# Kernel optimization log

Hardware: AMD Instinct MI355X
Metric: run time of the kernel (lower is better)

The kernel has to match this reference:

```python
import jax, jax.numpy as jnp
import numpy as np

B, A, N_IN, N_POINTS = 64, 256, 512, 2048


def _sq_cdist(u, v):
    # |u_i - v_j|^2 via expansion, abs() as in the torch original
    d = -2.0 * (u @ v.T) + (u * u).sum(1)[:, None] + (v * v).sum(1)[None, :]
    return jnp.abs(d)


def setup_inputs() -> dict:
    key = jax.random.key(0)
    k1, k2, k3, k4 = jax.random.split(key, 4)
    x = jax.random.normal(k1, (B, A, N_IN), dtype=jnp.float32)
    atom_mask = jax.random.bernoulli(k2, 0.8, (B, A))  # ragged valid-atom mask
    inducing_points = jax.random.normal(k3, (N_POINTS, N_IN), dtype=jnp.float32)
    gamma = (1.0 + 0.25 * jax.random.normal(k4, (N_IN,), dtype=jnp.float32)) * np.sqrt(N_IN).astype(np.float32)
    return {"x": x, "atom_mask": atom_mask, "inducing_points": inducing_points, "gamma": gamma}


def reference(x, atom_mask, inducing_points, gamma):
    b, a, n_in = x.shape
    m = atom_mask.astype(x.dtype)                      # [B, A]
    mf = m[..., None]                                  # [B, A, 1]
    n = m.sum()
    # masked mean / unbiased std over valid atoms (torch .std is ddof=1)
    mean = (x * mf).sum((0, 1)) / n                    # [n_in]
    var = (((x - mean) ** 2) * mf).sum((0, 1)) / (n - 1.0)
    std = jnp.sqrt(var) + 1e-5                         # [n_in]
    xn = (x - mean) / std * mf                         # zero out padded atoms

    g2 = gamma ** 2 + 0.001                            # [n_in]
    z = (xn / g2).reshape(b * a, n_in)                 # [N, n_in]
    zi = inducing_points / g2                          # [M, n_in]

    Kx = jnp.exp(-_sq_cdist(z, zi))                    # [N, M]
    Kind = jnp.exp(-_sq_cdist(zi, zi))                 # [M, M]
    Kinv = jnp.linalg.inv(Kind + 0.05 * jnp.eye(Kind.shape[0], dtype=x.dtype))

    t = Kx @ Kinv                                      # [N, M]
    x_new = ((t @ inducing_points) * std + mean).reshape(b, a, n_in) * mf
    var_out = (1.0 - (t * Kx).sum(-1)).reshape(b, a) * m
    return x_new, var_out
```

## Files before the change

### kernel.cpp

```cpp
#include <hip/hip_runtime.h>
#include <math.h>
#include <stdint.h>

namespace {

constexpr int NROW = 16384;
constexpr int NF   = 512;
constexpr int MIND = 2048;
constexpr float CC = 0.98f;

typedef _Float16 half8 __attribute__((ext_vector_type(8)));
typedef _Float16 half4v __attribute__((ext_vector_type(4)));
typedef float floatx4 __attribute__((ext_vector_type(4)));

__device__ __forceinline__ void gload16(const void* g, void* l) {
  __builtin_amdgcn_global_load_lds(
      (__attribute__((address_space(1))) void*)g,
      (__attribute__((address_space(3))) void*)l, 16, 0, 0);
}

#define MEMFENCE asm volatile("" ::: "memory")
#define GATE(N) asm volatile("s_waitcnt vmcnt(" #N ")" ::: "memory")

__global__ __launch_bounds__(256) void stats_kernel(
    const float* __restrict__ x, const int* __restrict__ mask,
    float* __restrict__ sum, float* __restrict__ sumsq, float* __restrict__ cnt)
{
  const int t = threadIdx.x;
  const int row0 = blockIdx.x * 64;
  float s0 = 0.f, s1 = 0.f, q0 = 0.f, q1 = 0.f, c = 0.f;
  for (int r = 0; r < 64; ++r) {
    const int row = row0 + r;
    const float m = (mask[row] != 0) ? 1.f : 0.f;
    const float v0 = x[(size_t)row * NF + t];
    const float v1 = x[(size_t)row * NF + t + 256];
    s0 += m * v0; q0 += m * v0 * v0;
    s1 += m * v1; q1 += m * v1 * v1;
    c += m;
  }
  atomicAdd(&sum[t], s0);        atomicAdd(&sum[t + 256], s1);
  atomicAdd(&sumsq[t], q0);      atomicAdd(&sumsq[t + 256], q1);
  if (t == 0) atomicAdd(cnt, c);
}

__global__ __launch_bounds__(256) void finalize_stats(
    const float* __restrict__ sum, const float* __restrict__ sumsq,
    const float* __restrict__ cnt, const float* __restrict__ gamma,
    float* __restrict__ meanv, float* __restrict__ stdv,
    float* __restrict__ zsv, float* __restrict__ giv)
{
  const int f = blockIdx.x * 256 + threadIdx.x;
  const float n = cnt[0];
  const float mu = sum[f] / n;
  const float var = (sumsq[f] - sum[f] * mu) / (n - 1.0f);
  const float sd = sqrtf(var) + 1e-5f;
  const float g = gamma[f];
  const float g2 = g * g + 0.001f;
  meanv[f] = mu;
  stdv[f]  = sd;
  zsv[f]   = 1.0f / (sd * g2);
  giv[f]   = 1.0f / g2;
}

__global__ __launch_bounds__(256) void make_z(
    const float* __restrict__ x, const int* __restrict__ mask,
    const float* __restrict__ ip, const float* __restrict__ meanv,
    const float* __restrict__ zsv, const float* __restrict__ giv,
    _Float16* __restrict__ Zh, _Float16* __restrict__ Zih,
    float* __restrict__ rnorm, float* __restrict__ cnorm)
{
  const int row = blockIdx.x;
  const int t = threadIdx.x;
  float v0, v1;
  if (row < NROW) {
    const float m = (mask[row] != 0) ? 1.f : 0.f;
    v0 = (x[(size_t)row * NF + t      ] - meanv[t      ]) * zsv[t      ] * m;
    v1 = (x[(size_t)row * NF + t + 256] - meanv[t + 256]) * zsv[t + 256] * m;
    const _Float16 h0 = (_Float16)v0, h1 = (_Float16)v1;
    Zh[(size_t)row * NF + t] = h0;
    Zh[(size_t)row * NF + t + 256] = h1;
    v0 = (float)h0; v1 = (float)h1;
  } else {
    const int r = row - NROW;
    v0 = ip[(size_t)r * NF + t      ] * giv[t      ];
    v1 = ip[(size_t)r * NF + t + 256] * giv[t + 256];
    const _Float16 h0 = (_Float16)v0, h1 = (_Float16)v1;
    Zih[(size_t)r * NF + t] = h0;
    Zih[(size_t)r * NF + t + 256] = h1;
    v0 = (float)h0; v1 = (float)h1;
  }
  float nrm = v0 * v0 + v1 * v1;
  #pragma unroll
  for (int off = 32; off; off >>= 1) nrm += __shfl_xor(nrm, off);
  __shared__ float red[4];
  if ((t & 63) == 0) red[t >> 6] = nrm;
  __syncthreads();
  if (t == 0) {
    const float s = red[0] + red[1] + red[2] + red[3];
    if (row < NROW) rnorm[row] = s; else cnorm[row - NROW] = s;
  }
}

__global__ __launch_bounds__(256) void ip_t16(
    const float* __restrict__ ip, _Float16* __restrict__ ipTh)
{
  __shared__ float T[64][65];
  const int j0 = blockIdx.x * 64;
  const int f0 = blockIdx.y * 64;
  const int t = threadIdx.x;
  #pragma unroll
  for (int l = 0; l < 16; ++l) {
    const int idx = t + l * 256;
    T[idx >> 6][idx & 63] = ip[(size_t)(j0 + (idx >> 6)) * NF + f0 + (idx & 63)];
  }
  __syncthreads();
  #pragma unroll
  for (int l = 0; l < 16; ++l) {
    const int idx = t + l * 256;
    const int fr = idx >> 6, jc = idx & 63;
    ipTh[(size_t)(f0 + fr) * MIND + j0 + jc] = (_Float16)T[jc][fr];
  }
}

template <int PASS>
__global__ __launch_bounds__(512, 2) void mfma_gemm256f(
    const _Float16* __restrict__ A, const _Float16* __restrict__ B, int K,
    const float* __restrict__ rn, const float* __restrict__ cn,
    _Float16* __restrict__ DKout, float* __restrict__ Cf,
    const _Float16* __restrict__ DK, const float* __restrict__ u,
    float* __restrict__ varacc,
    const float* __restrict__ colsumR, const float* __restrict__ stdv,
    const float* __restrict__ meanv, const int* __restrict__ mask)
{
  __shared__ __align__(16) _Float16 Asmem[4][256 * 32];
  __shared__ __align__(16) _Float16 Bsmem[4][256 * 32];

  const int tid = threadIdx.x;
  const int w = tid >> 6, L = tid & 63;
  const int wm = w >> 2, wn = w & 3;
  const int lq = L >> 4, lr = L & 15;
  int bn, bm;
  if constexpr (PASS == 0) {
    const int wgid = blockIdx.y * 8 + blockIdx.x;
    const int xcd = wgid & 7, q = wgid >> 3;
    bm = xcd + 8 * (q >> 3);
    bn = q & 7;
  } else if constexpr (PASS == 1) {
    const int wgid = blockIdx.y * 10 + blockIdx.x;
    const int xcd = wgid & 7, q = wgid >> 3;
    bm = xcd + 8 * (q / 10);
    bn = q % 10;
  } else {
    const int wgid = blockIdx.y * 8 + blockIdx.x;
    bm = wgid >> 3;
    bn = wgid & 7;
  }
  const int NT = K >> 5;

  const int srow  = tid >> 2;
  const int sslot = tid & 3;
  const int gslot = sslot ^ ((tid >> 3) & 3);
  const _Float16* Ag = A + (size_t)(bm * 256 + srow) * K + gslot * 8;
  const _Float16* Bg = B + (size_t)(bn * 256 + srow) * K + gslot * 8;
  const size_t rstride = (size_t)128 * K;
  const int ldst = srow * 32 + sslot * 8;

  const int fswz = (lq ^ ((lr >> 1) & 3)) * 8;
  const int aoff = (wm * 128 + lr) * 32 + fswz;
  const int boff = (wn * 64  + lr) * 32 + fswz;

  floatx4 acc[8][4] = {};

  auto stageA = [&](int t) {
    _Float16* dst = Asmem[t & 3] + ldst;
    const _Float16* src = Ag + (size_t)t * 32;
    gload16(src, dst);
    gload16(src + rstride, dst + 128 * 32);
  };
  auto stageB = [&](int t) {
    _Float16* dst = Bsmem[t & 3] + ldst;
    const _Float16* src = Bg + (size_t)t * 32;
    gload16(src, dst);
    gload16(src + rstride, dst + 128 * 32);
  };

  stageA(0); stageB(0);
  if (NT > 1) { stageA(1); stageB(1); }
  if (NT > 2) { stageA(2); stageB(2); }
  if (NT > 2)      { GATE(8); }
  else if (NT > 1) { GATE(4); }
  else             { GATE(0); }
  __builtin_amdgcn_s_barrier();
  MEMFENCE;

  for (int t = 0; t < NT; ++t) {
    const _Float16* As = Asmem[t & 3];
    const _Float16* Bs = Bsmem[t & 3];
    half8 af[4], bf[4], af2[4];

    #pragma unroll
    for (int mi = 0; mi < 4; ++mi) af[mi] = *(const half8*)&As[aoff + mi * 512];
    #pragma unroll
    for (int ni = 0; ni < 4; ++ni) bf[ni] = *(const half8*)&Bs[boff + ni * 512];
    if (t + 3 < NT) stageA(t + 3);
    MEMFENCE;
    __builtin_amdgcn_s_barrier();
    MEMFENCE;
    __builtin_amdgcn_s_setprio(1);
    #pragma unroll
    for (int mi = 0; mi < 4; ++mi)
      #pragma unroll
      for (int ni = 0; ni < 4; ++ni)
        acc[mi][ni] = __builtin_amdgcn_mfma_f32_16x16x32_f16(
            af[mi], bf[ni], acc[mi][ni], 0, 0, 0);
    __builtin_amdgcn_s_setprio(0);

    #pragma unroll
    for (int mi = 0; mi < 4; ++mi)
      af2[mi] = *(const half8*)&As[aoff + (mi + 4) * 512];
    if (t + 3 < NT) stageB(t + 3);
    if (t + 4 <= NT)      { GATE(8); }
    else if (t + 3 == NT) { GATE(4); }
    else if (t + 2 == NT) { GATE(0); }
    __builtin_amdgcn_s_barrier();
    MEMFENCE;
    __builtin_amdgcn_s_setprio(1);
    #pragma unroll
    for (int mi = 0; mi < 4; ++mi)
      #pragma unroll
      for (int ni = 0; ni < 4; ++ni)
        acc[mi + 4][ni] = __builtin_amdgcn_mfma_f32_16x16x32_f16(
            af2[mi], bf[ni], acc[mi + 4][ni], 0, 0, 0);
    __builtin_amdgcn_s_setprio(0);
  }

  const int grb = bm * 256 + wm * 128;
  const int gcb = bn * 256 + wn * 64;

  if constexpr (PASS == 0) {
    if (bm < NROW / 256) {
      #pragma unroll
      for (int mi = 0; mi < 8; ++mi)
        #pragma unroll
        for (int e = 0; e < 4; ++e) {
          const int gr = grb + mi * 16 + lq * 4 + e;
          const float rni = rn[gr];
          #pragma unroll
          for (int ni = 0; ni < 4; ++ni) {
            const int gc = gcb + ni * 16 + lr;
            const float d = rni + cn[gc] - 2.f * acc[mi][ni][e];
            DKout[(size_t)gr * MIND + gc] = (_Float16)(expf(-fabsf(d)) - CC);
          }
        }
    } else {
      #pragma unroll
      for (int mi = 0; mi < 8; ++mi)
        #pragma unroll
        for (int e = 0; e < 4; ++e) {
          const int gr = grb + mi * 16 + lq * 4 + e;
          const int gr2 = gr - NROW;
          const float rni = rn[gr];
          #pragma unroll
          for (int ni = 0; ni < 4; ++ni) {
            const int gc = gcb + ni * 16 + lr;
            const float d = rni + cn[gc] - 2.f * acc[mi][ni][e];
            float kx = expf(-fabsf(d));
            if (gr2 == gc) kx += 0.05f;
            Cf[(size_t)gr2 * MIND + gc] = kx;
          }
        }
    }
  } else if constexpr (PASS == 1) {
    if (bn < MIND / 256) {
      #pragma unroll
      for (int mi = 0; mi < 8; ++mi)
        #pragma unroll
        for (int e = 0; e < 4; ++e) {
          const int gr = grb + mi * 16 + lq * 4 + e;
          float partial = 0.f;
          #pragma unroll
          for (int ni = 0; ni < 4; ++ni) {
            const int gc = gcb + ni * 16 + lr;
            const float tv = acc[mi][ni][e] + CC * u[gc];
            partial += tv * (CC + (float)DK[(size_t)gr * MIND + gc]);
          }
          partial += __shfl_xor(partial, 1);
          partial += __shfl_xor(partial, 2);
          partial += __shfl_xor(partial, 4);
          partial += __shfl_xor(partial, 8);
          if (lr == 0) atomicAdd(&varacc[gr], partial);
        }
    } else {
      const int gcb3 = (bn - MIND / 256) * 256 + wn * 64;
      #pragma unroll
      for (int mi = 0; mi < 8; ++mi)
        #pragma unroll
        for (int e = 0; e < 4; ++e) {
          const int gr = grb + mi * 16 + lq * 4 + e;
          const float mrow = (mask[gr] != 0) ? 1.f : 0.f;
          #pragma unroll
          for (int ni = 0; ni < 4; ++ni) {
            const int gc3 = gcb3 + ni * 16 + lr;
            const float v = acc[mi][ni][e] + CC * colsumR[gc3];
            Cf[(size_t)gr * NF + gc3] = (v * stdv[gc3] + meanv[gc3]) * mrow;
          }
        }
    }
  } else {
    #pragma unroll
    for (int mi = 0; mi < 8; ++mi)
      #pragma unroll
      for (int e = 0; e < 4; ++e) {
        const int gr = grb + mi * 16 + lq * 4 + e;
        #pragma unroll
        for (int ni = 0; ni < 4; ++ni) {
          const int gc = gcb + ni * 16 + lr;
          DKout[(size_t)gr * MIND + gc] = (_Float16)acc[mi][ni][e];
        }
      }
  }
}


__global__ __launch_bounds__(256) void gj_diag(
    float* __restrict__ A, float* __restrict__ Pall, int k)
{
  const int o = k * 64;
  __shared__ float D[64][68];
  const int t = threadIdx.x;
  #pragma unroll
  for (int l = 0; l < 4; ++l) {
    const int v = t + l * 256;
    const int r = v >> 4, c4 = (v & 15) << 2;
    *(float4*)&D[r][c4] = *(const float4*)(A + (size_t)(o + r) * MIND + o + c4);
  }
  __syncthreads();
  const int i = t >> 2, c0 = (t & 3) * 16;
  for (int s = 0; s < 64; ++s) {
    const float p = 1.0f / D[s][s];
    if (t < 64 && t != s) D[s][t] *= p;
    __syncthreads();
    if (i != s) {
      const float f = D[i][s];
      #pragma unroll
      for (int c = c0; c < c0 + 16; c += 4) {
        float4 ds = *(const float4*)&D[s][c];
        float4 di = *(const float4*)&D[i][c];
        di.x -= f * ds.x; di.y -= f * ds.y; di.z -= f * ds.z; di.w -= f * ds.w;
        *(float4*)&D[i][c] = di;
      }
      if (s >= c0 && s < c0 + 16) D[i][s] = -f * p;
    }
    if (t == 0) D[s][s] = p;
    __syncthreads();
  }
  float* P = Pall + k * 4096;
  #pragma unroll
  for (int l = 0; l < 4; ++l) {
    const int v = t + l * 256;
    const int r = v >> 4, c4 = (v & 15) << 2;
    const float4 dv = *(const float4*)&D[r][c4];
    *(float4*)(P + r * 64 + c4) = dv;
    *(float4*)(A + (size_t)(o + r) * MIND + o + c4) = dv;
  }
}

__global__ __launch_bounds__(256) void gj_prep(
    const float* __restrict__ A, const float* __restrict__ Pall,
    float* __restrict__ CP, float* __restrict__ Bsave, int k)
{
  const int o = k * 64;
  const int t = threadIdx.x;
  if (blockIdx.x >= 32) {
    const int j0 = (blockIdx.x - 32) * 64;
    #pragma unroll
    for (int l = 0; l < 4; ++l) {
      const int v = t + l * 256;
      const int r = v >> 4, c4 = (v & 15) << 2;
      *(float4*)(Bsave + r * MIND + j0 + c4) =
          *(const float4*)(A + (size_t)(o + r) * MIND + j0 + c4);
    }
    return;
  }
  const int i0 = blockIdx.x * 64;
  if (i0 == o) return;
  const float* P = Pall + k * 4096;
  __shared__ float At[64][68];
  __shared__ float Pl[64][68];
  #pragma unroll
  for (int l = 0; l < 4; ++l) {
    const int v = t + l * 256;
    const int r = v >> 4, c4 = (v & 15) << 2;
    const float4 av = *(const float4*)(A + (size_t)(i0 + r) * MIND + o + c4);
    At[c4 + 0][r] = av.x; At[c4 + 1][r] = av.y;
    At[c4 + 2][r] = av.z; At[c4 + 3][r] = av.w;
    *(float4*)&Pl[r][c4] = *(const float4*)(P + r * 64 + c4);
  }
  __syncthreads();
  const int ty = t >> 4, tx = t & 15;
  float acc[4][4] = {};
  for (int s = 0; s < 64; ++s) {
    const float4 a4 = *(const float4*)&At[s][ty * 4];
    const float4 b4 = *(const float4*)&Pl[s][tx * 4];
    const float a[4] = {a4.x, a4.y, a4.z, a4.w};
    const float b[4] = {b4.x, b4.y, b4.z, b4.w};
    #pragma unroll
    for (int i = 0; i < 4; ++i)
      #pragma unroll
      for (int j = 0; j < 4; ++j) acc[i][j] += a[i] * b[j];
  }
  #pragma unroll
  for (int i = 0; i < 4; ++i) {
    float4 o4; o4.x = acc[i][0]; o4.y = acc[i][1]; o4.z = acc[i][2]; o4.w = acc[i][3];
    *(float4*)(CP + (i0 + ty * 4 + i) * 64 + tx * 4) = o4;
  }
}

__global__ __launch_bounds__(256) void gj_apply(
    float* __restrict__ A, float* __restrict__ Pall,
    const float* __restrict__ CP, const float* __restrict__ Bsave, int k)
{
  const int o = k * 64;
  const int i0 = blockIdx.y * 64, j0 = blockIdx.x * 64;
  const int t = threadIdx.x;

  if (i0 == o && j0 == o) return;

  if (j0 == o) {
    #pragma unroll
    for (int l = 0; l < 4; ++l) {
      const int v = t + l * 256;
      const int r = v >> 4, c4 = (v & 15) << 2;
      float4 x = *(const float4*)(CP + (i0 + r) * 64 + c4);
      x.x = -x.x; x.y = -x.y; x.z = -x.z; x.w = -x.w;
      *(float4*)(A + (size_t)(i0 + r) * MIND + o + c4) = x;
    }
    return;
  }

  __shared__ float S1[64 * 68];
  __shared__ float S2[64 * 68];
  #define DD(r, c) S1[(r) * 68 + (c)]

  const bool isrow = (i0 == o);
  const float* Lsrc = isrow ? (Pall + k * 4096) : (CP + i0 * 64);
  #pragma unroll
  for (int l = 0; l < 4; ++l) {
    const int v = t + l * 256;
    const int r = v >> 4, c4 = (v & 15) << 2;
    const float4 lv = *(const float4*)(Lsrc + r * 64 + c4);
    S1[(c4 + 0) * 68 + r] = lv.x; S1[(c4 + 1) * 68 + r] = lv.y;
    S1[(c4 + 2) * 68 + r] = lv.z; S1[(c4 + 3) * 68 + r] = lv.w;
    *(float4*)&S2[r * 68 + c4] = *(const float4*)(Bsave + r * MIND + j0 + c4);
  }
  __syncthreads();
  const int ty = t >> 4, tx = t & 15;
  float acc[4][4] = {};
  for (int s = 0; s < 64; ++s) {
    const float4 a4 = *(const float4*)&S1[s * 68 + ty * 4];
    const float4 b4 = *(const float4*)&S2[s * 68 + tx * 4];
    const float a[4] = {a4.x, a4.y, a4.z, a4.w};
    const float b[4] = {b4.x, b4.y, b4.z, b4.w};
    #pragma unroll
    for (int i = 0; i < 4; ++i)
      #pragma unroll
      for (int j = 0; j < 4; ++j) acc[i][j] += a[i] * b[j];
  }

  if (isrow) {
    #pragma unroll
    for (int i = 0; i < 4; ++i) {
      float4 o4; o4.x = acc[i][0]; o4.y = acc[i][1]; o4.z = acc[i][2]; o4.w = acc[i][3];
      *(float4*)(A + (size_t)(o + ty * 4 + i) * MIND + j0 + tx * 4) = o4;
    }
    return;
  }

  const bool isdiagnext = (i0 == o + 64) && (j0 == o + 64);
  if (!isdiagnext) {
    #pragma unroll
    for (int i = 0; i < 4; ++i) {
      float* cp = A + (size_t)(i0 + ty * 4 + i) * MIND + j0 + tx * 4;
      float4 cv = *(const float4*)cp;
      cv.x -= acc[i][0]; cv.y -= acc[i][1]; cv.z -= acc[i][2]; cv.w -= acc[i][3];
      *(float4*)cp = cv;
    }
    return;
  }

  __syncthreads();
  #pragma unroll
  for (int i = 0; i < 4; ++i) {
    const float4 cv = *(const float4*)(A + (size_t)(i0 + ty * 4 + i) * MIND + j0 + tx * 4);
    DD(ty * 4 + i, tx * 4 + 0) = cv.x - acc[i][0];
    DD(ty * 4 + i, tx * 4 + 1) = cv.y - acc[i][1];
    DD(ty * 4 + i, tx * 4 + 2) = cv.z - acc[i][2];
    DD(ty * 4 + i, tx * 4 + 3) = cv.w - acc[i][3];
  }
  __syncthreads();
  const int di = t >> 2, c0 = (t & 3) * 16;
  for (int s = 0; s < 64; ++s) {
    const float p = 1.0f / DD(s, s);
    if (t < 64 && t != s) DD(s, t) *= p;
    __syncthreads();
    if (di != s) {
      const float f = DD(di, s);
      #pragma unroll
      for (int c = c0; c < c0 + 16; c += 4) {
        float4 ds = *(const float4*)&DD(s, c);
        float4 dv = *(const float4*)&DD(di, c);
        dv.x -= f * ds.x; dv.y -= f * ds.y; dv.z -= f * ds.z; dv.w -= f * ds.w;
        *(float4*)&DD(di, c) = dv;
      }
      if (s >= c0 && s < c0 + 16) DD(di, s) = -f * p;
    }
    if (t == 0) DD(s, s) = p;
    __syncthreads();
  }
  float* Pn = Pall + (k + 1) * 4096;
  #pragma unroll
  for (int l = 0; l < 4; ++l) {
    const int v = t + l * 256;
    const int r = v >> 4, c4 = (v & 15) << 2;
    const float4 dv = *(const float4*)&DD(r, c4);
    *(float4*)(Pn + r * 64 + c4) = dv;
    *(float4*)(A + (size_t)(i0 + r) * MIND + j0 + c4) = dv;
  }
  #undef DD
}

__global__ __launch_bounds__(256) void rowsum_cast(
    const float* __restrict__ Ai, float* __restrict__ u,
    _Float16* __restrict__ Kih)
{
  const int row = blockIdx.x * 4 + (threadIdx.x >> 6);
  const int lane = threadIdx.x & 63;
  const float* src = Ai + (size_t)row * MIND;
  _Float16* dst = Kih + (size_t)row * MIND;
  float s = 0.f;
  #pragma unroll
  for (int it = 0; it < 8; ++it) {
    const int c = it * 256 + lane * 4;
    const float4 v = *(const float4*)(src + c);
    s += v.x + v.y + v.z + v.w;
    half4v h; h.x = (_Float16)v.x; h.y = (_Float16)v.y;
    h.z = (_Float16)v.z; h.w = (_Float16)v.w;
    *(half4v*)(dst + c) = h;
  }
  #pragma unroll
  for (int off = 32; off; off >>= 1) s += __shfl_xor(s, off);
  if (lane == 0) u[row] = s;
}

__global__ __launch_bounds__(256) void colsum_u(
    const float* __restrict__ ip, const float* __restrict__ u,
    float* __restrict__ cs)
{
  const int b = blockIdx.x;
  const int t = threadIdx.x;
  float s0 = 0.f, s1 = 0.f;
  for (int r = 0; r < 64; ++r) {
    const int row = b * 64 + r;
    const float uk = u[row];
    s0 += uk * ip[(size_t)row * NF + t];
    s1 += uk * ip[(size_t)row * NF + t + 256];
  }
  atomicAdd(&cs[t], s0); atomicAdd(&cs[t + 256], s1);
}

__global__ __launch_bounds__(256) void var_finalize(
    const float* __restrict__ varacc, const int* __restrict__ mask,
    float* __restrict__ outv)
{
  const int i = blockIdx.x * 256 + threadIdx.x;
  const float m = (mask[i] != 0) ? 1.f : 0.f;
  outv[i] = (1.0f - varacc[i]) * m;
}

}

extern "C" void kernel_launch(void* const* d_in, const int* in_sizes, int n_in,
                              void* d_out, int out_size, void* d_ws, size_t ws_size,
                              hipStream_t stream)
{
  (void)in_sizes; (void)n_in; (void)out_size; (void)ws_size;
  const float* x     = (const float*)d_in[0];
  const int*   mask  = (const int*)d_in[1];
  const float* ip    = (const float*)d_in[2];
  const float* gamma = (const float*)d_in[3];
  float* out = (float*)d_out;

  float* w       = (float*)d_ws;
  float* sum     = w;
  float* sumsq   = w + 512;
  float* cnt     = w + 1024;
  float* varacc  = w + 1536;
  float* colsumR = w + 17920;
  float* meanv   = w + 18432;
  float* stdv    = w + 18944;
  float* zsv     = w + 19456;
  float* giv     = w + 19968;
  float* rnorm   = w + 20480;
  float* cnorm   = w + 36864;
  float* u       = w + 38912;
  float* Ai      = w + 40960;
  _Float16* ipTh = (_Float16*)(w + 4235264);
  float* Pall    = w + 5283840;
  float* CP      = w + 5414912;
  float* Bsave   = w + 5545984;
  _Float16* hb   = (_Float16*)(w + 5677056);
  _Float16* Zh   = hb;
  _Float16* Zih  = hb + 8388608;
  _Float16* DK   = hb + 9437184;
  _Float16* Kih  = hb + 42991616;
  _Float16* Rt   = hb + 47185920;

  hipMemsetAsync(w, 0, 18432 * sizeof(float), stream);

  stats_kernel<<<256, 256, 0, stream>>>(x, mask, sum, sumsq, cnt);
  finalize_stats<<<2, 256, 0, stream>>>(sum, sumsq, cnt, gamma, meanv, stdv, zsv, giv);
  make_z<<<NROW + MIND, 256, 0, stream>>>(x, mask, ip, meanv, zsv, giv, Zh, Zih, rnorm, cnorm);
  ip_t16<<<dim3(MIND / 64, NF / 64), 256, 0, stream>>>(ip, ipTh);

  mfma_gemm256f<0><<<dim3(MIND / 256, (NROW + MIND) / 256), 512, 0, stream>>>(
      Zh, Zih, NF, rnorm, cnorm,
      DK, Ai, nullptr, nullptr, nullptr, nullptr, nullptr, nullptr, nullptr);

  gj_diag<<<1, 256, 0, stream>>>(Ai, Pall, 0);
  gj_prep<<<64, 256, 0, stream>>>(Ai, Pall, CP, Bsave, 0);
  for (int k = 0; k < 32; ++k) {
    gj_apply<<<dim3(32, 32), 256, 0, stream>>>(Ai, Pall, CP, Bsave, k);
    if (k < 31) gj_prep<<<64, 256, 0, stream>>>(Ai, Pall, CP, Bsave, k + 1);
  }

  rowsum_cast<<<MIND / 4, 256, 0, stream>>>(Ai, u, Kih);
  mfma_gemm256f<2><<<dim3(8, 2), 512, 0, stream>>>(
      ipTh, Kih, MIND, nullptr, nullptr,
      Rt, nullptr, nullptr, nullptr, nullptr, nullptr, nullptr, nullptr, nullptr);
  colsum_u<<<MIND / 64, 256, 0, stream>>>(ip, u, colsumR);

  mfma_gemm256f<1><<<dim3((MIND + NF) / 256, NROW / 256), 512, 0, stream>>>(
      DK, Kih, MIND, nullptr, nullptr,
      nullptr, out, DK, u, varacc, colsumR, stdv, meanv, mask);

  var_finalize<<<NROW / 256, 256, 0, stream>>>(varacc, mask, out + (size_t)NROW * NF);
}
```

Before: 2.032 ms.

## Fuse Gauss-Jordan prep into apply with tile flags and merge small kernels

Folds the next step's pivot-panel prep into each Gauss-Jordan apply launch. Extra blocks spin on per-tile release/acquire flags until the tiles they need are ready, and the CP/Bsave buffers are double-buffered so reads and writes do not collide. This removes 31 separate prep launches and their serialization. It also folds stats finalization and the ip transpose into make_z, and folds the colsum into the small GEMM launch as extra blocks. The spin-wait relies on the producer blocks being scheduled alongside or before the waiting ones, which risks stalls or deadlock.

```diff
diff --git a/kernel.cpp b/kernel.cpp
--- a/kernel.cpp
+++ b/kernel.cpp
@@ -43,47 +43,65 @@
   if (t == 0) atomicAdd(cnt, c);
 }
 
-__global__ __launch_bounds__(256) void finalize_stats(
-    const float* __restrict__ sum, const float* __restrict__ sumsq,
-    const float* __restrict__ cnt, const float* __restrict__ gamma,
-    float* __restrict__ meanv, float* __restrict__ stdv,
-    float* __restrict__ zsv, float* __restrict__ giv)
-{
-  const int f = blockIdx.x * 256 + threadIdx.x;
-  const float n = cnt[0];
-  const float mu = sum[f] / n;
-  const float var = (sumsq[f] - sum[f] * mu) / (n - 1.0f);
-  const float sd = sqrtf(var) + 1e-5f;
-  const float g = gamma[f];
-  const float g2 = g * g + 0.001f;
-  meanv[f] = mu;
-  stdv[f]  = sd;
-  zsv[f]   = 1.0f / (sd * g2);
-  giv[f]   = 1.0f / g2;
-}
-
 __global__ __launch_bounds__(256) void make_z(
     const float* __restrict__ x, const int* __restrict__ mask,
-    const float* __restrict__ ip, const float* __restrict__ meanv,
-    const float* __restrict__ zsv, const float* __restrict__ giv,
+    const float* __restrict__ ip, const float* __restrict__ sum,
+    const float* __restrict__ sumsq, const float* __restrict__ cnt,
+    const float* __restrict__ gamma,
     _Float16* __restrict__ Zh, _Float16* __restrict__ Zih,
-    float* __restrict__ rnorm, float* __restrict__ cnorm)
-{
+    float* __restrict__ rnorm, float* __restrict__ cnorm,
+    float* __restrict__ meanv, float* __restrict__ stdv,
+    _Float16* __restrict__ ipTh)
+{
+  __shared__ float T[64][65];
   const int row = blockIdx.x;
   const int t = threadIdx.x;
+
+  if (row >= NROW + MIND) {
+    const int idx2 = row - (NROW + MIND);
+    const int j0 = (idx2 & 31) * 64, f0 = (idx2 >> 5) * 64;
+    #pragma unroll
+    for (int l = 0; l < 16; ++l) {
+      const int idx = t + l * 256;
+      T[idx >> 6][idx & 63] = ip[(size_t)(j0 + (idx >> 6)) * NF + f0 + (idx & 63)];
+    }
+    __syncthreads();
+    #pragma unroll
+    for (int l = 0; l < 16; ++l) {
+      const int idx = t + l * 256;
+      const int fr = idx >> 6, jc = idx & 63;
+      ipTh[(size_t)(f0 + fr) * MIND + j0 + jc] = (_Float16)T[jc][fr];
+    }
+    return;
+  }
+
+  const float n = cnt[0];
+  float mu[2], zs[2], gi[2];
+  #pragma unroll
+  for (int h = 0; h < 2; ++h) {
+    const int f = t + h * 256;
+    const float m0 = sum[f] / n;
+    const float var = (sumsq[f] - sum[f] * m0) / (n - 1.0f);
+    const float sd = sqrtf(var) + 1e-5f;
+    const float g = gamma[f];
+    const float g2 = g * g + 0.001f;
+    mu[h] = m0; zs[h] = 1.0f / (sd * g2); gi[h] = 1.0f / g2;
+    if (row == 0) { meanv[f] = m0; stdv[f] = sd; }
+  }
+
   float v0, v1;
   if (row < NROW) {
     const float m = (mask[row] != 0) ? 1.f : 0.f;
-    v0 = (x[(size_t)row * NF + t      ] - meanv[t      ]) * zsv[t      ] * m;
-    v1 = (x[(size_t)row * NF + t + 256] - meanv[t + 256]) * zsv[t + 256] * m;
+    v0 = (x[(size_t)row * NF + t      ] - mu[0]) * zs[0] * m;
+    v1 = (x[(size_t)row * NF + t + 256] - mu[1]) * zs[1] * m;
     const _Float16 h0 = (_Float16)v0, h1 = (_Float16)v1;
     Zh[(size_t)row * NF + t] = h0;
     Zh[(size_t)row * NF + t + 256] = h1;
     v0 = (float)h0; v1 = (float)h1;
   } else {
     const int r = row - NROW;
-    v0 = ip[(size_t)r * NF + t      ] * giv[t      ];
-    v1 = ip[(size_t)r * NF + t + 256] * giv[t + 256];
+    v0 = ip[(size_t)r * NF + t      ] * gi[0];
+    v1 = ip[(size_t)r * NF + t + 256] * gi[1];
     const _Float16 h0 = (_Float16)v0, h1 = (_Float16)v1;
     Zih[(size_t)r * NF + t] = h0;
     Zih[(size_t)r * NF + t + 256] = h1;
@@ -92,33 +110,11 @@
   float nrm = v0 * v0 + v1 * v1;
   #pragma unroll
   for (int off = 32; off; off >>= 1) nrm += __shfl_xor(nrm, off);
-  __shared__ float red[4];
-  if ((t & 63) == 0) red[t >> 6] = nrm;
+  if ((t & 63) == 0) T[0][t >> 6] = nrm;
   __syncthreads();
   if (t == 0) {
-    const float s = red[0] + red[1] + red[2] + red[3];
+    const float s = T[0][0] + T[0][1] + T[0][2] + T[0][3];
     if (row < NROW) rnorm[row] = s; else cnorm[row - NROW] = s;
-  }
-}
-
-__global__ __launch_bounds__(256) void ip_t16(
-    const float* __restrict__ ip, _Float16* __restrict__ ipTh)
-{
-  __shared__ float T[64][65];
-  const int j0 = blockIdx.x * 64;
-  const int f0 = blockIdx.y * 64;
-  const int t = threadIdx.x;
-  #pragma unroll
-  for (int l = 0; l < 16; ++l) {
-    const int idx = t + l * 256;
-    T[idx >> 6][idx & 63] = ip[(size_t)(j0 + (idx >> 6)) * NF + f0 + (idx & 63)];
-  }
-  __syncthreads();
-  #pragma unroll
-  for (int l = 0; l < 16; ++l) {
-    const int idx = t + l * 256;
-    const int fr = idx >> 6, jc = idx & 63;
-    ipTh[(size_t)(f0 + fr) * MIND + j0 + jc] = (_Float16)T[jc][fr];
   }
 }
 
@@ -152,6 +148,14 @@
     bn = q % 10;
   } else {
     const int wgid = blockIdx.y * 8 + blockIdx.x;
+    if (wgid >= 16) {
+      const int r0 = (wgid - 16) * 64;
+      float s = 0.f;
+      for (int r = 0; r < 64; ++r)
+        s += u[r0 + r] * rn[(size_t)(r0 + r) * NF + tid];
+      atomicAdd(&varacc[tid], s);
+      return;
+    }
     bm = wgid >> 3;
     bn = wgid & 7;
   }
@@ -416,34 +420,104 @@
   }
 }
 
-__global__ __launch_bounds__(256) void gj_apply(
+__global__ __launch_bounds__(256) void gj_fused(
     float* __restrict__ A, float* __restrict__ Pall,
-    const float* __restrict__ CP, const float* __restrict__ Bsave, int k)
+    const float* __restrict__ CPr, const float* __restrict__ BSr,
+    float* __restrict__ CPw, float* __restrict__ BSw,
+    int* __restrict__ fP, int* __restrict__ ttile, int k)
 {
   const int o = k * 64;
-  const int i0 = blockIdx.y * 64, j0 = blockIdx.x * 64;
   const int t = threadIdx.x;
-
-  if (i0 == o && j0 == o) return;
-
-  if (j0 == o) {
+  __shared__ float S1[64 * 68];
+  __shared__ float S2[64 * 68];
+  #define DD(r, c) S1[(r) * 68 + (c)]
+
+  if (blockIdx.x >= 1024) {
+    const int pb = blockIdx.x - 1024;
+    const int o2 = o + 64, g2 = o2 >> 6;
+    if (pb >= 32) {
+      const int jg = pb - 32, j0 = jg * 64;
+      if (t == 0)
+        while (__hip_atomic_load(&ttile[g2 * 32 + jg], __ATOMIC_ACQUIRE,
+                                 __HIP_MEMORY_SCOPE_AGENT) < k + 1)
+          __builtin_amdgcn_s_sleep(8);
+      __syncthreads();
+      #pragma unroll
+      for (int l = 0; l < 4; ++l) {
+        const int v = t + l * 256;
+        const int r = v >> 4, c4 = (v & 15) << 2;
+        *(float4*)(BSw + r * MIND + j0 + c4) =
+            *(const float4*)(A + (size_t)(o2 + r) * MIND + j0 + c4);
+      }
+      return;
+    }
+    const int i0 = pb * 64;
+    if (i0 == o2) return;
+    if (t == 0) {
+      while (__hip_atomic_load(fP, __ATOMIC_ACQUIRE,
+                               __HIP_MEMORY_SCOPE_AGENT) < k + 2)
+        __builtin_amdgcn_s_sleep(8);
+      while (__hip_atomic_load(&ttile[pb * 32 + g2], __ATOMIC_ACQUIRE,
+                               __HIP_MEMORY_SCOPE_AGENT) < k + 1)
+        __builtin_amdgcn_s_sleep(8);
+    }
+    __syncthreads();
+    const float* P = Pall + (size_t)(k + 1) * 4096;
     #pragma unroll
     for (int l = 0; l < 4; ++l) {
       const int v = t + l * 256;
       const int r = v >> 4, c4 = (v & 15) << 2;
-      float4 x = *(const float4*)(CP + (i0 + r) * 64 + c4);
+      const float4 av = *(const float4*)(A + (size_t)(i0 + r) * MIND + o2 + c4);
+      S1[(c4 + 0) * 68 + r] = av.x; S1[(c4 + 1) * 68 + r] = av.y;
+      S1[(c4 + 2) * 68 + r] = av.z; S1[(c4 + 3) * 68 + r] = av.w;
+      *(float4*)&S2[r * 68 + c4] = *(const float4*)(P + r * 64 + c4);
+    }
+    __syncthreads();
+    const int ty = t >> 4, tx = t & 15;
+    float acc[4][4] = {};
+    for (int s = 0; s < 64; ++s) {
+      const float4 a4 = *(const float4*)&S1[s * 68 + ty * 4];
+      const float4 b4 = *(const float4*)&S2[s * 68 + tx * 4];
+      const float a[4] = {a4.x, a4.y, a4.z, a4.w};
+      const float b[4] = {b4.x, b4.y, b4.z, b4.w};
+      #pragma unroll
+      for (int i = 0; i < 4; ++i)
+        #pragma unroll
+        for (int j = 0; j < 4; ++j) acc[i][j] += a[i] * b[j];
+    }
+    #pragma unroll
+    for (int i = 0; i < 4; ++i) {
+      float4 o4; o4.x = acc[i][0]; o4.y = acc[i][1]; o4.z = acc[i][2]; o4.w = acc[i][3];
+      *(float4*)(CPw + (i0 + ty * 4 + i) * 64 + tx * 4) = o4;
+    }
+    return;
+  }
+
+  const int ig = blockIdx.x >> 5, jg = blockIdx.x & 31;
+  const int i0 = ig * 64, j0 = jg * 64;
+
+  if (i0 == o && j0 == o) return;
+
+  if (j0 == o) {
+    #pragma unroll
+    for (int l = 0; l < 4; ++l) {
+      const int v = t + l * 256;
+      const int r = v >> 4, c4 = (v & 15) << 2;
+      float4 x = *(const float4*)(CPr + (i0 + r) * 64 + c4);
       x.x = -x.x; x.y = -x.y; x.z = -x.z; x.w = -x.w;
       *(float4*)(A + (size_t)(i0 + r) * MIND + o + c4) = x;
     }
+    __syncthreads();
+    if (t == 0) {
+      __threadfence();
+      __hip_atomic_store(&ttile[ig * 32 + jg], k + 1, __ATOMIC_RELEASE,
+                         __HIP_MEMORY_SCOPE_AGENT);
+    }
     return;
   }
 
-  __shared__ float S1[64 * 68];
-  __shared__ float S2[64 * 68];
-  #define DD(r, c) S1[(r) * 68 + (c)]
-
   const bool isrow = (i0 == o);
-  const float* Lsrc = isrow ? (Pall + k * 4096) : (CP + i0 * 64);
+  const float* Lsrc = isrow ? (Pall + (size_t)k * 4096) : (CPr + i0 * 64);
   #pragma unroll
   for (int l = 0; l < 4; ++l) {
     const int v = t + l * 256;
@@ -451,7 +525,7 @@
     const float4 lv = *(const float4*)(Lsrc + r * 64 + c4);
     S1[(c4 + 0) * 68 + r] = lv.x; S1[(c4 + 1) * 68 + r] = lv.y;
     S1[(c4 + 2) * 68 + r] = lv.z; S1[(c4 + 3) * 68 + r] = lv.w;
-    *(float4*)&S2[r * 68 + c4] = *(const float4*)(Bsave + r * MIND + j0 + c4);
+    *(float4*)&S2[r * 68 + c4] = *(const float4*)(BSr + r * MIND + j0 + c4);
   }
   __syncthreads();
   const int ty = t >> 4, tx = t & 15;
@@ -473,6 +547,12 @@
       float4 o4; o4.x = acc[i][0]; o4.y = acc[i][1]; o4.z = acc[i][2]; o4.w = acc[i][3];
       *(float4*)(A + (size_t)(o + ty * 4 + i) * MIND + j0 + tx * 4) = o4;
     }
+    __syncthreads();
+    if (t == 0) {
+      __threadfence();
+      __hip_atomic_store(&ttile[ig * 32 + jg], k + 1, __ATOMIC_RELEASE,
+                         __HIP_MEMORY_SCOPE_AGENT);
+    }
     return;
   }
 
@@ -484,6 +564,12 @@
       float4 cv = *(const float4*)cp;
       cv.x -= acc[i][0]; cv.y -= acc[i][1]; cv.z -= acc[i][2]; cv.w -= acc[i][3];
       *(float4*)cp = cv;
+    }
+    __syncthreads();
+    if (t == 0) {
+      __threadfence();
+      __hip_atomic_store(&ttile[ig * 32 + jg], k + 1, __ATOMIC_RELEASE,
+                         __HIP_MEMORY_SCOPE_AGENT);
     }
     return;
   }
@@ -517,7 +603,7 @@
     if (t == 0) DD(s, s) = p;
     __syncthreads();
   }
-  float* Pn = Pall + (k + 1) * 4096;
+  float* Pn = Pall + (size_t)(k + 1) * 4096;
   #pragma unroll
   for (int l = 0; l < 4; ++l) {
     const int v = t + l * 256;
@@ -525,6 +611,14 @@
     const float4 dv = *(const float4*)&DD(r, c4);
     *(float4*)(Pn + r * 64 + c4) = dv;
     *(float4*)(A + (size_t)(i0 + r) * MIND + j0 + c4) = dv;
+  }
+  __syncthreads();
+  if (t == 0) {
+    __threadfence();
+    __hip_atomic_store(&ttile[ig * 32 + jg], k + 1, __ATOMIC_RELEASE,
+                       __HIP_MEMORY_SCOPE_AGENT);
+    __hip_atomic_store(fP, k + 2, __ATOMIC_RELEASE,
+                       __HIP_MEMORY_SCOPE_AGENT);
   }
   #undef DD
 }
@@ -552,22 +646,6 @@
   if (lane == 0) u[row] = s;
 }
 
-__global__ __launch_bounds__(256) void colsum_u(
-    const float* __restrict__ ip, const float* __restrict__ u,
-    float* __restrict__ cs)
-{
-  const int b = blockIdx.x;
-  const int t = threadIdx.x;
-  float s0 = 0.f, s1 = 0.f;
-  for (int r = 0; r < 64; ++r) {
-    const int row = b * 64 + r;
-    const float uk = u[row];
-    s0 += uk * ip[(size_t)row * NF + t];
-    s1 += uk * ip[(size_t)row * NF + t + 256];
-  }
-  atomicAdd(&cs[t], s0); atomicAdd(&cs[t + 256], s1);
-}
-
 __global__ __launch_bounds__(256) void var_finalize(
     const float* __restrict__ varacc, const int* __restrict__ mask,
     float* __restrict__ outv)
@@ -594,17 +672,19 @@
   float* sum     = w;
   float* sumsq   = w + 512;
   float* cnt     = w + 1024;
-  float* varacc  = w + 1536;
-  float* colsumR = w + 17920;
-  float* meanv   = w + 18432;
-  float* stdv    = w + 18944;
-  float* zsv     = w + 19456;
-  float* giv     = w + 19968;
-  float* rnorm   = w + 20480;
-  float* cnorm   = w + 36864;
-  float* u       = w + 38912;
+  int*   fP      = (int*)(w + 1028);
+  int*   ttile   = (int*)(w + 1056);
+  float* varacc  = w + 2560;
+  float* colsumR = w + 18944;
+  float* meanv   = w + 19456;
+  float* stdv    = w + 19968;
+  float* u       = w + 20480;
+  float* rnorm   = w + 22528;
+  float* cnorm   = w + 38912;
   float* Ai      = w + 40960;
   _Float16* ipTh = (_Float16*)(w + 4235264);
+  float* CP2     = w + 4759552;
+  float* Bs2     = w + 4890624;
   float* Pall    = w + 5283840;
   float* CP      = w + 5414912;
   float* Bsave   = w + 5545984;
@@ -615,29 +695,32 @@
   _Float16* Kih  = hb + 42991616;
   _Float16* Rt   = hb + 47185920;
 
-  hipMemsetAsync(w, 0, 18432 * sizeof(float), stream);
+  hipMemsetAsync(w, 0, 19456 * sizeof(float), stream);
 
   stats_kernel<<<256, 256, 0, stream>>>(x, mask, sum, sumsq, cnt);
-  finalize_stats<<<2, 256, 0, stream>>>(sum, sumsq, cnt, gamma, meanv, stdv, zsv, giv);
-  make_z<<<NROW + MIND, 256, 0, stream>>>(x, mask, ip, meanv, zsv, giv, Zh, Zih, rnorm, cnorm);
-  ip_t16<<<dim3(MIND / 64, NF / 64), 256, 0, stream>>>(ip, ipTh);
+  make_z<<<NROW + MIND + 256, 256, 0, stream>>>(
+      x, mask, ip, sum, sumsq, cnt, gamma,
+      Zh, Zih, rnorm, cnorm, meanv, stdv, ipTh);
 
   mfma_gemm256f<0><<<dim3(MIND / 256, (NROW + MIND) / 256), 512, 0, stream>>>(
       Zh, Zih, NF, rnorm, cnorm,
       DK, Ai, nullptr, nullptr, nullptr, nullptr, nullptr, nullptr, nullptr);
 
+  float* CPb[2] = {CP, CP2};
+  float* BSb[2] = {Bsave, Bs2};
   gj_diag<<<1, 256, 0, stream>>>(Ai, Pall, 0);
-  gj_prep<<<64, 256, 0, stream>>>(Ai, Pall, CP, Bsave, 0);
+  gj_prep<<<64, 256, 0, stream>>>(Ai, Pall, CPb[0], BSb[0], 0);
   for (int k = 0; k < 32; ++k) {
-    gj_apply<<<dim3(32, 32), 256, 0, stream>>>(Ai, Pall, CP, Bsave, k);
-    if (k < 31) gj_prep<<<64, 256, 0, stream>>>(Ai, Pall, CP, Bsave, k + 1);
+    const int nb = (k < 31) ? 1088 : 1024;
+    gj_fused<<<nb, 256, 0, stream>>>(
+        Ai, Pall, CPb[k & 1], BSb[k & 1],
+        CPb[(k + 1) & 1], BSb[(k + 1) & 1], fP, ttile, k);
   }
 
   rowsum_cast<<<MIND / 4, 256, 0, stream>>>(Ai, u, Kih);
-  mfma_gemm256f<2><<<dim3(8, 2), 512, 0, stream>>>(
-      ipTh, Kih, MIND, nullptr, nullptr,
-      Rt, nullptr, nullptr, nullptr, nullptr, nullptr, nullptr, nullptr, nullptr);
-  colsum_u<<<MIND / 64, 256, 0, stream>>>(ip, u, colsumR);
+  mfma_gemm256f<2><<<dim3(8, 6), 512, 0, stream>>>(
+      ipTh, Kih, MIND, ip, nullptr,
+      Rt, nullptr, nullptr, u, colsumR, nullptr, nullptr, nullptr, nullptr);
 
   mfma_gemm256f<1><<<dim3((MIND + NF) / 256, NROW / 256), 512, 0, stream>>>(
       DK, Kih, MIND, nullptr, nullptr,
```

Result: slower. 2.612 ms (+28.5%).
